# Kernel optimization log

Hardware: AMD Instinct MI355X
Metric: run time of the kernel (lower is better)

## Reference

```python
import jax, jax.numpy as jnp
import numpy as np

H_OUT = 2
H_DIM = 256
V_DIM = 128
Q_DIM = 128


def setup_inputs() -> dict:
    key = jax.random.key(0)
    ks = jax.random.split(key, 10)
    B, NV, NQ = 8, 128, 512
    s = 0.02
    return {
        "v": jax.random.normal(ks[0], (B, NV, V_DIM), dtype=jnp.float32),
        "q": jax.random.normal(ks[1], (B, NQ, Q_DIM), dtype=jnp.float32),
        "Wv": jax.random.normal(ks[2], (V_DIM, H_DIM * H_OUT), dtype=jnp.float32) * s,
        "bv": jax.random.normal(ks[3], (H_DIM * H_OUT,), dtype=jnp.float32) * s,
        "Wq": jax.random.normal(ks[4], (Q_DIM, H_DIM * H_OUT), dtype=jnp.float32) * s,
        "bq": jax.random.normal(ks[5], (H_DIM * H_OUT,), dtype=jnp.float32) * s,
        "wa": jax.random.normal(ks[6], (H_DIM,), dtype=jnp.float32) * s,
        "ba": jax.random.normal(ks[7], (), dtype=jnp.float32) * s,
        "Wo": jax.random.normal(ks[8], (H_OUT * H_DIM, H_DIM), dtype=jnp.float32) * s,
        "bo": jax.random.normal(ks[9], (H_DIM,), dtype=jnp.float32) * s,
    }


def reference(v, q, Wv, bv, Wq, bq, wa, ba, Wo, bo):
    B, NV, _ = v.shape
    NQ = q.shape[1]
    # projections -> (B, N, h_out, h_dim)
    v_ = (v @ Wv + bv).reshape(B, NV, H_OUT, H_DIM)
    q_ = (q @ Wq + bq).reshape(B, NQ, H_OUT, H_DIM)
    # att_proj on the outer product, without materializing the joint tensor:
    # score[b,h,i,j] = sum_d v_[b,i,h,d]*q_[b,j,h,d]*wa[d] + ba
    score = jnp.einsum("bihd,bjhd,d->bhij", v_, q_, wa) + ba
    att = jax.nn.softmax(score, axis=2)  # softmax over num_v (dim=2), as in torch
    # weighted sum: head[b,h,d] = sum_{i,j} att[b,h,i,j]*v_[b,i,h,d]*q_[b,j,h,d]
    ctx = jnp.einsum("bhij,bjhd->bihd", att, q_)
    head = jnp.einsum("bihd,bihd->bhd", ctx, v_)
    fused = head.reshape(B, H_OUT * H_DIM) @ Wo + bo
    att_out = att.reshape(B, H_OUT, NV * NQ, 1)  # matches torch's final view+unsqueeze
    return fused, att_out
```

## Files before the change

### kernel.cpp

```cpp
#include <hip/hip_runtime.h>
#include <math.h>

#define B_  8
#define NV_ 128
#define NQ_ 512
#define KD_ 128
#define P_  512
#define H_  2
#define D_  256

typedef unsigned short ushort_t;
typedef unsigned int   uint_t;
typedef __attribute__((ext_vector_type(8))) short bf16x8;
typedef __attribute__((ext_vector_type(4))) float f32x4;

#define QBF_OFF  0
#define VWA_OFF  (4u<<20)
#define VT_OFF   (5u<<20)
#define HEAD_OFF (7u<<20)
#define WVT_OFF  (8u<<20)
#define WQT_OFF  ((8u<<20) + (128u<<10))

__device__ __forceinline__ ushort_t f2b(float f) {
    uint_t u = __float_as_uint(f);
    uint_t r = (u + 0x7FFFu + ((u >> 16) & 1u)) >> 16;
    return (ushort_t)r;
}
__device__ __forceinline__ float b2f(ushort_t u) {
    return __uint_as_float(((uint_t)u) << 16);
}

extern "C" __global__ void __launch_bounds__(256) prep_kernel(
    const float* __restrict__ Wv, const float* __restrict__ Wq,
    char* __restrict__ ws)
{
    ushort_t* wvt = (ushort_t*)(ws + WVT_OFF);
    ushort_t* wqt = (ushort_t*)(ws + WQT_OFF);
    float*    head = (float*)(ws + HEAD_OFF);

    __shared__ ushort_t lt[128][34];

    const int bid = blockIdx.x, t = threadIdx.x;
    const int wsel = bid >> 4, cb = bid & 15, c0 = cb * 32;
    const float* W = wsel ? Wq : Wv;
    ushort_t*   WT = wsel ? wqt : wvt;

    if (t < 128) head[bid * 128 + t] = 0.f;

#pragma unroll
    for (int it = 0; it < 4; ++it) {
        const int idx = it * 256 + t;
        const int k = idx >> 3, cq = (idx & 7) * 4;
        const float4 f = *(const float4*)&W[(size_t)k * P_ + c0 + cq];
        uint_t* dst = (uint_t*)&lt[k][cq];
        dst[0] = (uint_t)f2b(f.x) | ((uint_t)f2b(f.y) << 16);
        dst[1] = (uint_t)f2b(f.z) | ((uint_t)f2b(f.w) << 16);
    }
    __syncthreads();

#pragma unroll
    for (int it = 0; it < 2; ++it) {
        const int idx = it * 256 + t;
        const int c = idx & 31, kg = idx >> 5;
        bf16x8 u;
#pragma unroll
        for (int r = 0; r < 8; ++r) u[r] = (short)lt[kg * 8 + r][c];
        *(bf16x8*)&WT[(size_t)(c0 + c) * 128 + kg * 8] = u;
    }
}

extern "C" __global__ void __launch_bounds__(256) proj_kernel(
    const float* __restrict__ v, const float* __restrict__ q,
    const float* __restrict__ bv, const float* __restrict__ bq,
    const float* __restrict__ wa, char* __restrict__ ws)
{
    ushort_t* qbf = (ushort_t*)(ws + QBF_OFF);
    ushort_t* vwa = (ushort_t*)(ws + VWA_OFF);
    ushort_t* vT  = (ushort_t*)(ws + VT_OFF);

    __shared__ __align__(16) char ldsb[32 * 264 * 2];
    ushort_t (*A)[136] = (ushort_t (*)[136])ldsb;
    ushort_t (*O)[264] = (ushort_t (*)[264])ldsb;

    const int bid = blockIdx.x, t = threadIdx.x;
    const int w = t >> 6, l = t & 63, l15 = l & 15, lg = l >> 4;

    const bool is_v = (bid < 32);
    int b, r0;
    const float* src; const float* bias;
    if (is_v) { b = bid >> 2;                r0 = (bid & 3) * 32;  src = v + (size_t)(b * NV_ + r0) * KD_; bias = bv; }
    else      { const int tq = bid - 32; b = tq >> 4; r0 = (tq & 15) * 32; src = q + (size_t)(b * NQ_ + r0) * KD_; bias = bq; }
    const ushort_t* WT = (const ushort_t*)(ws + (is_v ? WVT_OFF : WQT_OFF));

#pragma unroll
    for (int it = 0; it < 4; ++it) {
        const int idx = it * 256 + t;
        const int row = idx >> 5, kq = (idx & 31) * 4;
        const float4 f = *(const float4*)&src[(size_t)row * KD_ + kq];
        uint_t* dst = (uint_t*)&A[row][kq];
        dst[0] = (uint_t)f2b(f.x) | ((uint_t)f2b(f.y) << 16);
        dst[1] = (uint_t)f2b(f.z) | ((uint_t)f2b(f.w) << 16);
    }
    __syncthreads();

    const int n0 = w * 128;
    f32x4 acc[2][8];
#pragma unroll
    for (int mf = 0; mf < 2; ++mf)
#pragma unroll
        for (int nf = 0; nf < 8; ++nf) acc[mf][nf] = (f32x4){0.f, 0.f, 0.f, 0.f};

#pragma unroll
    for (int ks = 0; ks < 4; ++ks) {
        const int ko = ks * 32 + lg * 8;
        bf16x8 Af[2];
#pragma unroll
        for (int mf = 0; mf < 2; ++mf)
            Af[mf] = *(const bf16x8*)&A[mf * 16 + l15][ko];
        bf16x8 Bf[8];
#pragma unroll
        for (int nf = 0; nf < 8; ++nf)
            Bf[nf] = *(const bf16x8*)&WT[(size_t)(n0 + nf * 16 + l15) * 128 + ko];
#pragma unroll
        for (int mf = 0; mf < 2; ++mf)
#pragma unroll
            for (int nf = 0; nf < 8; ++nf)
                acc[mf][nf] = __builtin_amdgcn_mfma_f32_16x16x32_bf16(Af[mf], Bf[nf], acc[mf][nf], 0, 0, 0);
    }
    __syncthreads();

    for (int p = 0; p < 2; ++p) {
        if ((w >> 1) == p) {
            const int nbase = (w & 1) * 128;
#pragma unroll
            for (int mf = 0; mf < 2; ++mf)
#pragma unroll
                for (int nf = 0; nf < 8; ++nf) {
                    const int m = mf * 16 + lg * 4;
                    const int n = nbase + nf * 16 + l15;
                    const float bcol = bias[p * 256 + n];
#pragma unroll
                    for (int r = 0; r < 4; ++r)
                        O[m + r][n] = f2b(acc[mf][nf][r] + bcol);
                }
        }
        __syncthreads();
#pragma unroll
        for (int it = 0; it < 4; ++it) {
            const int idx = it * 256 + t;
            const int row = idx >> 5, d0 = (idx & 31) * 8;
            const bf16x8 u = *(const bf16x8*)&O[row][d0];
            if (is_v) {
                const float4 wa0 = *(const float4*)&wa[d0];
                const float4 wa1 = *(const float4*)&wa[d0 + 4];
                bf16x8 s;
                s[0] = (short)f2b(b2f((ushort_t)u[0]) * wa0.x);
                s[1] = (short)f2b(b2f((ushort_t)u[1]) * wa0.y);
                s[2] = (short)f2b(b2f((ushort_t)u[2]) * wa0.z);
                s[3] = (short)f2b(b2f((ushort_t)u[3]) * wa0.w);
                s[4] = (short)f2b(b2f((ushort_t)u[4]) * wa1.x);
                s[5] = (short)f2b(b2f((ushort_t)u[5]) * wa1.y);
                s[6] = (short)f2b(b2f((ushort_t)u[6]) * wa1.z);
                s[7] = (short)f2b(b2f((ushort_t)u[7]) * wa1.w);
                *(bf16x8*)&vwa[((size_t)(b * 2 + p) * 128 + r0 + row) * 256 + d0] = s;
            } else {
                *(bf16x8*)&qbf[((size_t)(b * 2 + p) * 512 + r0 + row) * 256 + d0] = u;
            }
        }
        if (is_v) {
#pragma unroll
            for (int it = 0; it < 4; ++it) {
                const int d  = (t & 63) + it * 64;
                const int ic = t >> 6;
                bf16x8 u;
#pragma unroll
                for (int r = 0; r < 8; ++r) u[r] = (short)O[ic * 8 + r][d];
                *(bf16x8*)&vT[((size_t)(b * 2 + p) * 256 + d) * 128 + r0 + ic * 8] = u;
            }
        }
        __syncthreads();
    }
}

extern "C" __global__ void __launch_bounds__(256, 1) att_kernel(
    char* __restrict__ ws, float* __restrict__ out)
{
    const ushort_t* qbf = (const ushort_t*)(ws + QBF_OFF);
    const ushort_t* vwa = (const ushort_t*)(ws + VWA_OFF);
    const ushort_t* vT  = (const ushort_t*)(ws + VT_OFF);
    float*          head = (float*)(ws + HEAD_OFF);
    float*          att_out = out + B_ * D_;

    __shared__ ushort_t q_lds[32][264];
    __shared__ ushort_t p_lds[32][136];
    __shared__ float wmax[4][32];
    __shared__ float wsum[4][32];

    const int t  = threadIdx.x;
    const int w  = t >> 6;
    const int l  = t & 63;
    const int l15 = l & 15, lg = l >> 4;

    const int bid = blockIdx.x;
    const int jt  = bid & 15;
    const int h   = (bid >> 4) & 1;
    const int b   = bid >> 5;
    const int j0  = jt * 32;
    const size_t bh = (size_t)(b * H_ + h);

    const ushort_t* vwa_p = vwa + bh * 128 * 256;
    const ushort_t* vT_p  = vT  + bh * 256 * 128;
    const ushort_t* qp    = qbf + (bh * 512 + j0) * 256;

    const ushort_t* a0 = vwa_p + (size_t)(w * 32 + l15) * 256 + lg * 8;
    const ushort_t* a1 = a0 + 16 * 256;
    bf16x8 Afr0[8], Afr1[8];
#pragma unroll
    for (int ks = 0; ks < 8; ++ks) {
        Afr0[ks] = *(const bf16x8*)(a0 + ks * 32);
        Afr1[ks] = *(const bf16x8*)(a1 + ks * 32);
    }

    bf16x8 Vfr[4][4];
#pragma unroll
    for (int nb = 0; nb < 4; ++nb) {
        const ushort_t* vb = vT_p + (size_t)(w * 64 + nb * 16 + l15) * 128 + lg * 8;
#pragma unroll
        for (int ks = 0; ks < 4; ++ks)
            Vfr[nb][ks] = *(const bf16x8*)(vb + ks * 32);
    }

    for (int c = t; c < 1024; c += 256) {
        const int row = c >> 5, c8 = (c & 31) * 8;
        *(bf16x8*)&q_lds[row][c8] = *(const bf16x8*)&qp[(size_t)row * 256 + c8];
    }
    __syncthreads();

    const ushort_t* bq0 = &q_lds[l15][lg * 8];
    const ushort_t* bq1 = &q_lds[l15 + 16][lg * 8];

    f32x4 acc[2][2];
#pragma unroll
    for (int mb = 0; mb < 2; ++mb)
#pragma unroll
        for (int nb = 0; nb < 2; ++nb) acc[mb][nb] = (f32x4){0.f, 0.f, 0.f, 0.f};

#pragma unroll
    for (int ks = 0; ks < 8; ++ks) {
        const int ko = ks * 32;
        const bf16x8 B0 = *(const bf16x8*)(bq0 + ko);
        const bf16x8 B1 = *(const bf16x8*)(bq1 + ko);
        acc[0][0] = __builtin_amdgcn_mfma_f32_16x16x32_bf16(Afr0[ks], B0, acc[0][0], 0, 0, 0);
        acc[0][1] = __builtin_amdgcn_mfma_f32_16x16x32_bf16(Afr0[ks], B1, acc[0][1], 0, 0, 0);
        acc[1][0] = __builtin_amdgcn_mfma_f32_16x16x32_bf16(Afr1[ks], B0, acc[1][0], 0, 0, 0);
        acc[1][1] = __builtin_amdgcn_mfma_f32_16x16x32_bf16(Afr1[ks], B1, acc[1][1], 0, 0, 0);
    }

    float mx[2];
#pragma unroll
    for (int nb = 0; nb < 2; ++nb) {
        float m = acc[0][nb][0];
#pragma unroll
        for (int mb = 0; mb < 2; ++mb)
#pragma unroll
            for (int r = 0; r < 4; ++r) m = fmaxf(m, acc[mb][nb][r]);
        m = fmaxf(m, __shfl_xor(m, 16));
        m = fmaxf(m, __shfl_xor(m, 32));
        mx[nb] = m;
    }
    if (l < 16) { wmax[w][l] = mx[0]; wmax[w][l + 16] = mx[1]; }
    __syncthreads();

    float cm[2];
#pragma unroll
    for (int nb = 0; nb < 2; ++nb) {
        const int jl = nb * 16 + l15;
        cm[nb] = fmaxf(fmaxf(wmax[0][jl], wmax[1][jl]), fmaxf(wmax[2][jl], wmax[3][jl]));
    }

    float sm[2] = {0.f, 0.f};
#pragma unroll
    for (int mb = 0; mb < 2; ++mb)
#pragma unroll
        for (int nb = 0; nb < 2; ++nb)
#pragma unroll
            for (int r = 0; r < 4; ++r) {
                const float e = __expf(acc[mb][nb][r] - cm[nb]);
                acc[mb][nb][r] = e;
                sm[nb] += e;
            }
#pragma unroll
    for (int nb = 0; nb < 2; ++nb) {
        sm[nb] += __shfl_xor(sm[nb], 16);
        sm[nb] += __shfl_xor(sm[nb], 32);
    }
    if (l < 16) { wsum[w][l] = sm[0]; wsum[w][l + 16] = sm[1]; }
    __syncthreads();

    float cinv[2];
#pragma unroll
    for (int nb = 0; nb < 2; ++nb) {
        const int jl = nb * 16 + l15;
        cinv[nb] = 1.f / (wsum[0][jl] + wsum[1][jl] + wsum[2][jl] + wsum[3][jl]);
    }

    float* attp = att_out + (bh * 128) * 512 + j0;
#pragma unroll
    for (int mb = 0; mb < 2; ++mb) {
        const int il = w * 32 + mb * 16 + lg * 4;
#pragma unroll
        for (int nb = 0; nb < 2; ++nb) {
            const int jl = nb * 16 + l15;
            float p0 = acc[mb][nb][0] * cinv[nb];
            float p1 = acc[mb][nb][1] * cinv[nb];
            float p2 = acc[mb][nb][2] * cinv[nb];
            float p3 = acc[mb][nb][3] * cinv[nb];
            attp[(size_t)(il + 0) * 512 + jl] = p0;
            attp[(size_t)(il + 1) * 512 + jl] = p1;
            attp[(size_t)(il + 2) * 512 + jl] = p2;
            attp[(size_t)(il + 3) * 512 + jl] = p3;
            const uint_t u01 = (uint_t)f2b(p0) | ((uint_t)f2b(p1) << 16);
            const uint_t u23 = (uint_t)f2b(p2) | ((uint_t)f2b(p3) << 16);
            *(uint_t*)&p_lds[jl][il + 0] = u01;
            *(uint_t*)&p_lds[jl][il + 2] = u23;
        }
    }
    __syncthreads();

    f32x4 wacc[2][4];
#pragma unroll
    for (int mb = 0; mb < 2; ++mb)
#pragma unroll
        for (int nb = 0; nb < 4; ++nb) wacc[mb][nb] = (f32x4){0.f, 0.f, 0.f, 0.f};

    const ushort_t* pb0 = &p_lds[l15][lg * 8];
    const ushort_t* pb1 = &p_lds[l15 + 16][lg * 8];

#pragma unroll
    for (int ks = 0; ks < 4; ++ks) {
        const int ko = ks * 32;
        const bf16x8 PA0 = *(const bf16x8*)(pb0 + ko);
        const bf16x8 PA1 = *(const bf16x8*)(pb1 + ko);
#pragma unroll
        for (int nb = 0; nb < 4; ++nb) {
            wacc[0][nb] = __builtin_amdgcn_mfma_f32_16x16x32_bf16(PA0, Vfr[nb][ks], wacc[0][nb], 0, 0, 0);
            wacc[1][nb] = __builtin_amdgcn_mfma_f32_16x16x32_bf16(PA1, Vfr[nb][ks], wacc[1][nb], 0, 0, 0);
        }
    }

    float hd[4] = {0.f, 0.f, 0.f, 0.f};
#pragma unroll
    for (int nb = 0; nb < 4; ++nb) {
        const int d = w * 64 + nb * 16 + l15;
#pragma unroll
        for (int mb = 0; mb < 2; ++mb)
#pragma unroll
            for (int r = 0; r < 4; ++r) {
                const int jl = mb * 16 + lg * 4 + r;
                hd[nb] = fmaf(wacc[mb][nb][r], b2f(q_lds[jl][d]), hd[nb]);
            }
        hd[nb] += __shfl_xor(hd[nb], 16);
        hd[nb] += __shfl_xor(hd[nb], 32);
    }
    if (l < 16) {
        float* hp = head + bh * 256 + w * 64 + l;
        atomicAdd(hp +  0, hd[0]);
        atomicAdd(hp + 16, hd[1]);
        atomicAdd(hp + 32, hd[2]);
        atomicAdd(hp + 48, hd[3]);
    }
}

extern "C" __global__ void __launch_bounds__(256) out_kernel(
    const float* __restrict__ Wo, const float* __restrict__ bo,
    const char* __restrict__ ws, float* __restrict__ out)
{
    const float* head = (const float*)(ws + HEAD_OFF);
    __shared__ __align__(16) float hs[512];
    __shared__ float ored[4][64];

    const int bid = blockIdx.x, t = threadIdx.x;
    const int b = bid >> 2, cg = bid & 3;
    const int col = cg * 64 + (t & 63), kq = t >> 6;

    hs[t]       = head[(size_t)b * 512 + t];
    hs[t + 256] = head[(size_t)b * 512 + t + 256];
    __syncthreads();

    float acc = 0.f;
    const int kbeg = kq * 128;
    for (int k = kbeg; k < kbeg + 128; k += 4) {
        const float4 hk = *(const float4*)&hs[k];
        acc = fmaf(hk.x, Wo[(size_t)(k+0)*256 + col], acc);
        acc = fmaf(hk.y, Wo[(size_t)(k+1)*256 + col], acc);
        acc = fmaf(hk.z, Wo[(size_t)(k+2)*256 + col], acc);
        acc = fmaf(hk.w, Wo[(size_t)(k+3)*256 + col], acc);
    }
    ored[kq][t & 63] = acc;
    __syncthreads();
    if (t < 64) {
        const float r = ored[0][t] + ored[1][t] + ored[2][t] + ored[3][t] + bo[col];
        out[(size_t)b * 256 + col] = r;
    }
}

extern "C" void kernel_launch(void* const* d_in, const int* in_sizes, int n_in,
                              void* d_out, int out_size, void* d_ws, size_t ws_size,
                              hipStream_t stream)
{
    const float* v  = (const float*)d_in[0];
    const float* q  = (const float*)d_in[1];
    const float* Wv = (const float*)d_in[2];
    const float* bv = (const float*)d_in[3];
    const float* Wq = (const float*)d_in[4];
    const float* bq = (const float*)d_in[5];
    const float* wa = (const float*)d_in[6];
    const float* Wo = (const float*)d_in[8];
    const float* bo = (const float*)d_in[9];
    float* out = (float*)d_out;
    char*  ws  = (char*)d_ws;

    hipLaunchKernelGGL(prep_kernel, dim3(32),  dim3(256), 0, stream, Wv, Wq, ws);
    hipLaunchKernelGGL(proj_kernel, dim3(160), dim3(256), 0, stream, v, q, bv, bq, wa, ws);
    hipLaunchKernelGGL(att_kernel,  dim3(256), dim3(256), 0, stream, ws, out);
    hipLaunchKernelGGL(out_kernel,  dim3(32),  dim3(256), 0, stream, Wo, bo, ws, out);
}
```

Baseline: 101.1 us.

## Fuse output projection into attention kernel via per-block partial matvec and atomics

Removes the separate output-projection kernel and the global head buffer. Each attention block reduces its head slice into shared memory, multiplies it by its slice of Wo, and atomically accumulates into the output, which prep_kernel pre-initializes with the bias. This saves a kernel launch and a global round trip, but adds redundant Wo reads across the 16 j-tiles and more float atomics on the output.

Result: no change. 101.9 us (+0.8%).

```diff
diff --git a/kernel.cpp b/kernel.cpp
--- a/kernel.cpp
+++ b/kernel.cpp
@@ -17,7 +17,6 @@
 #define QBF_OFF  0
 #define VWA_OFF  (4u<<20)
 #define VT_OFF   (5u<<20)
-#define HEAD_OFF (7u<<20)
 #define WVT_OFF  (8u<<20)
 #define WQT_OFF  ((8u<<20) + (128u<<10))
 
@@ -32,11 +31,11 @@
 
 extern "C" __global__ void __launch_bounds__(256) prep_kernel(
     const float* __restrict__ Wv, const float* __restrict__ Wq,
-    char* __restrict__ ws)
+    const float* __restrict__ bo, char* __restrict__ ws,
+    float* __restrict__ out)
 {
     ushort_t* wvt = (ushort_t*)(ws + WVT_OFF);
     ushort_t* wqt = (ushort_t*)(ws + WQT_OFF);
-    float*    head = (float*)(ws + HEAD_OFF);
 
     __shared__ ushort_t lt[128][34];
 
@@ -45,7 +44,7 @@
     const float* W = wsel ? Wq : Wv;
     ushort_t*   WT = wsel ? wqt : wvt;
 
-    if (t < 128) head[bid * 128 + t] = 0.f;
+    if (bid < 8) out[(size_t)bid * 256 + t] = bo[t];
 
 #pragma unroll
     for (int it = 0; it < 4; ++it) {
@@ -183,18 +182,19 @@
 }
 
 extern "C" __global__ void __launch_bounds__(256, 1) att_kernel(
-    char* __restrict__ ws, float* __restrict__ out)
+    char* __restrict__ ws, const float* __restrict__ Wo,
+    float* __restrict__ out)
 {
     const ushort_t* qbf = (const ushort_t*)(ws + QBF_OFF);
     const ushort_t* vwa = (const ushort_t*)(ws + VWA_OFF);
     const ushort_t* vT  = (const ushort_t*)(ws + VT_OFF);
-    float*          head = (float*)(ws + HEAD_OFF);
     float*          att_out = out + B_ * D_;
 
     __shared__ ushort_t q_lds[32][264];
     __shared__ ushort_t p_lds[32][136];
     __shared__ float wmax[4][32];
     __shared__ float wsum[4][32];
+    __shared__ float head_lds[256];
 
     const int t  = threadIdx.x;
     const int w  = t >> 6;
@@ -363,45 +363,19 @@
         hd[nb] += __shfl_xor(hd[nb], 32);
     }
     if (l < 16) {
-        float* hp = head + bh * 256 + w * 64 + l;
-        atomicAdd(hp +  0, hd[0]);
-        atomicAdd(hp + 16, hd[1]);
-        atomicAdd(hp + 32, hd[2]);
-        atomicAdd(hp + 48, hd[3]);
-    }
-}
-
-extern "C" __global__ void __launch_bounds__(256) out_kernel(
-    const float* __restrict__ Wo, const float* __restrict__ bo,
-    const char* __restrict__ ws, float* __restrict__ out)
-{
-    const float* head = (const float*)(ws + HEAD_OFF);
-    __shared__ __align__(16) float hs[512];
-    __shared__ float ored[4][64];
-
-    const int bid = blockIdx.x, t = threadIdx.x;
-    const int b = bid >> 2, cg = bid & 3;
-    const int col = cg * 64 + (t & 63), kq = t >> 6;
-
-    hs[t]       = head[(size_t)b * 512 + t];
-    hs[t + 256] = head[(size_t)b * 512 + t + 256];
-    __syncthreads();
-
-    float acc = 0.f;
-    const int kbeg = kq * 128;
-    for (int k = kbeg; k < kbeg + 128; k += 4) {
-        const float4 hk = *(const float4*)&hs[k];
-        acc = fmaf(hk.x, Wo[(size_t)(k+0)*256 + col], acc);
-        acc = fmaf(hk.y, Wo[(size_t)(k+1)*256 + col], acc);
-        acc = fmaf(hk.z, Wo[(size_t)(k+2)*256 + col], acc);
-        acc = fmaf(hk.w, Wo[(size_t)(k+3)*256 + col], acc);
-    }
-    ored[kq][t & 63] = acc;
-    __syncthreads();
-    if (t < 64) {
-        const float r = ored[0][t] + ored[1][t] + ored[2][t] + ored[3][t] + bo[col];
-        out[(size_t)b * 256 + col] = r;
-    }
+        head_lds[w * 64 + l     ] = hd[0];
+        head_lds[w * 64 + l + 16] = hd[1];
+        head_lds[w * 64 + l + 32] = hd[2];
+        head_lds[w * 64 + l + 48] = hd[3];
+    }
+    __syncthreads();
+
+    const float* Wop = Wo + (size_t)(h * 256) * 256 + t;
+    float oacc = 0.f;
+#pragma unroll 16
+    for (int d = 0; d < 256; ++d)
+        oacc = fmaf(head_lds[d], Wop[(size_t)d * 256], oacc);
+    atomicAdd(&out[(size_t)b * 256 + t], oacc);
 }
 
 extern "C" void kernel_launch(void* const* d_in, const int* in_sizes, int n_in,
@@ -420,8 +394,7 @@
     float* out = (float*)d_out;
     char*  ws  = (char*)d_ws;
 
-    hipLaunchKernelGGL(prep_kernel, dim3(32),  dim3(256), 0, stream, Wv, Wq, ws);
+    hipLaunchKernelGGL(prep_kernel, dim3(32),  dim3(256), 0, stream, Wv, Wq, bo, ws, out);
     hipLaunchKernelGGL(proj_kernel, dim3(160), dim3(256), 0, stream, v, q, bv, bq, wa, ws);
-    hipLaunchKernelGGL(att_kernel,  dim3(256), dim3(256), 0, stream, ws, out);
-    hipLaunchKernelGGL(out_kernel,  dim3(32),  dim3(256), 0, stream, Wo, bo, ws, out);
-}
+    hipLaunchKernelGGL(att_kernel,  dim3(256), dim3(256), 0, stream, ws, Wo, out);
+}
```
